# Optimization experiments

Measured on AMD Instinct MI355X. Metric: run time of the kernel, lower is better.

Reference implementation:

```python
import jax, jax.numpy as jnp
import numpy as np

D_MODEL = 1024
NUM_HEADS = 16
D_K = D_MODEL // NUM_HEADS


def setup_inputs() -> dict:
    key = jax.random.key(0)
    ks = jax.random.split(key, 12)
    B, S, D = 2, 2048, D_MODEL
    s = 1.0 / np.sqrt(D)
    inp = {
        "Q": jax.random.normal(ks[0], (B, S, D), jnp.float32),
        "K": jax.random.normal(ks[1], (B, S, D), jnp.float32),
        "V": jax.random.normal(ks[2], (B, S, D), jnp.float32),
        "Wq": jax.random.normal(ks[3], (D, D), jnp.float32) * s,
        "bq": jax.random.normal(ks[4], (D,), jnp.float32) * s,
        "Wk": jax.random.normal(ks[5], (D, D), jnp.float32) * s,
        "bk": jax.random.normal(ks[6], (D,), jnp.float32) * s,
        "Wv": jax.random.normal(ks[7], (D, D), jnp.float32) * s,
        "bv": jax.random.normal(ks[8], (D,), jnp.float32) * s,
        "Wo": jax.random.normal(ks[9], (D, D), jnp.float32) * s,
        "bo": jax.random.normal(ks[10], (D,), jnp.float32) * s,
    }
    return inp


def _split_heads(x, B, S):
    # [B, S, D] -> [B, H, S, d_k]
    return x.reshape(B, S, NUM_HEADS, D_K).transpose(0, 2, 1, 3)


def reference(Q, K, V, Wq, bq, Wk, bk, Wv, bv, Wo, bo):
    B, S, D = Q.shape
    # torch nn.Linear: y = x @ W.T + b
    q = _split_heads(Q @ Wq.T + bq, B, S)
    k = _split_heads(K @ Wk.T + bk, B, S)
    v = _split_heads(V @ Wv.T + bv, B, S)
    scale = 1.0 / np.sqrt(D_K).astype(np.float32)
    # [B, H, S, S] attention scores (materialized, as in the original)
    scores = jnp.einsum('bhqd,bhkd->bhqk', q, k) * scale
    probs = jax.nn.softmax(scores, axis=-1)
    out = jnp.einsum('bhqk,bhkd->bhqd', probs, v)
    out = out.transpose(0, 2, 1, 3).reshape(B, S, D)
    return out @ Wo.T + bo
```

## Files before the change

### kernel.cpp

```cpp
#include <hip/hip_runtime.h>
#include <hip/hip_bf16.h>

#define S_LEN   2048
#define NHEADS  16
#define DKH     64
#define DMODEL  1024
#define NBATCH  2

typedef __bf16 bf16x8 __attribute__((ext_vector_type(8)));
typedef __bf16 bf16x4 __attribute__((ext_vector_type(4)));
typedef float  f32x4  __attribute__((ext_vector_type(4)));

typedef __attribute__((address_space(3))) void       lds_void;
typedef const __attribute__((address_space(1))) void glob_void;

__device__ __forceinline__ void glds16(const void* g, void* l) {
    __builtin_amdgcn_global_load_lds((glob_void*)g, (lds_void*)l, 16, 0, 0);
}

struct CvtArgs {
    const float* src[7];
    __bf16*      dst[7];
    int          n[7];
};

__global__ __launch_bounds__(256)
void cvt_all_k(CvtArgs a)
{
    const int t = blockIdx.y;
    const size_t i = ((size_t)blockIdx.x * 256 + threadIdx.x) * 8;
    if ((int)i >= a.n[t]) return;
    const float* s = a.src[t];
    f32x4 lo = *(const f32x4*)(s + i);
    f32x4 hi = *(const f32x4*)(s + i + 4);
    bf16x8 r;
#pragma unroll
    for (int k = 0; k < 4; ++k) { r[k] = (__bf16)lo[k]; r[4 + k] = (__bf16)hi[k]; }
    *(bf16x8*)(a.dst[t] + i) = r;
}

__device__ __forceinline__ void gemm_core(
    const __bf16* __restrict__ A, const __bf16* __restrict__ W,
    int m0, int n0, int K,
    __bf16 (*As)[32], __bf16 (*Ws)[32], f32x4 acc[4][4])
{
    const int tid  = threadIdx.x;
    const int lane = tid & 63;
    const int wv   = tid >> 6;
    const int l15  = lane & 15;
    const int quad = lane >> 4;
    const int wm   = wv >> 1;
    const int wn   = wv & 1;
    const int grow = lane >> 2;
    const int gcol = (lane & 3) * 8;

    const __bf16* ag0 = A + (size_t)(m0 + wv * 32 + grow) * K + gcol;
    const __bf16* ag1 = A + (size_t)(m0 + wv * 32 + 16 + grow) * K + gcol;
    const __bf16* wg0 = W + (size_t)(n0 + wv * 32 + grow) * K + gcol;
    const __bf16* wg1 = W + (size_t)(n0 + wv * 32 + 16 + grow) * K + gcol;
    void* al0 = &As[wv * 32][0];
    void* al1 = &As[wv * 32 + 16][0];
    void* wl0 = &Ws[wv * 32][0];
    void* wl1 = &Ws[wv * 32 + 16][0];

    for (int k0 = 0;;) {
        __syncthreads();
        glds16(ag0 + k0, al0);
        glds16(ag1 + k0, al1);
        glds16(wg0 + k0, wl0);
        glds16(wg1 + k0, wl1);
        __syncthreads();

        bf16x8 af[4], wf[4];
#pragma unroll
        for (int i = 0; i < 4; ++i)
            af[i] = *(const bf16x8*)&As[wm * 64 + i * 16 + l15][quad * 8];
#pragma unroll
        for (int j = 0; j < 4; ++j)
            wf[j] = *(const bf16x8*)&Ws[wn * 64 + j * 16 + l15][quad * 8];
#pragma unroll
        for (int i = 0; i < 4; ++i)
#pragma unroll
            for (int j = 0; j < 4; ++j)
                acc[i][j] = __builtin_amdgcn_mfma_f32_16x16x32_bf16(af[i], wf[j], acc[i][j], 0, 0, 0);

        k0 += 32;
        if (k0 >= K) break;
    }
}

struct GArgs {
    const __bf16* A[3];
    const __bf16* W[3];
    const float*  bias[3];
    __bf16*       out[3];
};

__global__ __launch_bounds__(256)
void gemm_qkv(GArgs g, int z_off)
{
    __shared__ __align__(16) __bf16 As[128][32];
    __shared__ __align__(16) __bf16 Ws[128][32];

    const int fid = blockIdx.x;
    const int z   = (fid >> 8) + z_off;
    const int f8  = fid & 255;
    int m0, n0;
    if (z == 2) { m0 = (f8 & 7) * 128;  n0 = (f8 >> 3) * 128; }
    else        { m0 = (f8 & 31) * 128; n0 = (f8 >> 5) * 128; }

    f32x4 acc[4][4];
#pragma unroll
    for (int i = 0; i < 4; ++i)
#pragma unroll
        for (int j = 0; j < 4; ++j) acc[i][j] = (f32x4){0.f, 0.f, 0.f, 0.f};

    gemm_core(g.A[z], g.W[z], m0, n0, DMODEL, As, Ws, acc);

    const int lane = threadIdx.x & 63;
    const int wv   = threadIdx.x >> 6;
    const int l15  = lane & 15;
    const int quad = lane >> 4;
    const int wm   = wv >> 1;
    const int wn   = wv & 1;
    const float* bias = g.bias[z];
    __bf16* out = g.out[z];
    const float oscale = (z == 0) ? 0.125f : 1.0f;

#pragma unroll
    for (int j = 0; j < 4; ++j) {
        const int col = n0 + wn * 64 + j * 16 + l15;
        const float bcol = (z == 2) ? 0.f : bias[col];
#pragma unroll
        for (int i = 0; i < 4; ++i) {
#pragma unroll
            for (int r = 0; r < 4; ++r) {
                const int row = m0 + wm * 64 + i * 16 + quad * 4 + r;
                size_t idx;
                float v = acc[i][j][r];
                if (z == 2) {
                    const int h = row >> 6, d = row & (DKH - 1);
                    const int b = col >> 11, s = col & (S_LEN - 1);
                    v += bias[row];
                    idx = ((size_t)(b * NHEADS + h) * DKH + d) * S_LEN + s;
                } else {
                    const int b = row >> 11, s = row & (S_LEN - 1);
                    const int h = col >> 6, d = col & (DKH - 1);
                    v = (v + bcol) * oscale;
                    idx = ((size_t)(b * NHEADS + h) * S_LEN + s) * DKH + d;
                }
                out[idx] = (__bf16)v;
            }
        }
    }
}

__global__ __launch_bounds__(256)
void gemm_out(const __bf16* __restrict__ A, const __bf16* __restrict__ W,
              const float* __restrict__ bias, float* __restrict__ out)
{
    __shared__ __align__(16) __bf16 As[128][32];
    __shared__ __align__(16) __bf16 Ws[128][32];

    const int fid = blockIdx.x;
    const int m0 = (fid & 31) * 128;
    const int n0 = (fid >> 5) * 128;

    f32x4 acc[4][4];
#pragma unroll
    for (int i = 0; i < 4; ++i)
#pragma unroll
        for (int j = 0; j < 4; ++j) acc[i][j] = (f32x4){0.f, 0.f, 0.f, 0.f};

    gemm_core(A, W, m0, n0, DMODEL, As, Ws, acc);

    const int lane = threadIdx.x & 63;
    const int wv   = threadIdx.x >> 6;
    const int l15  = lane & 15;
    const int quad = lane >> 4;
    const int wm   = wv >> 1;
    const int wn   = wv & 1;

#pragma unroll
    for (int j = 0; j < 4; ++j) {
        const int col = n0 + wn * 64 + j * 16 + l15;
        const float bv = bias[col];
#pragma unroll
        for (int i = 0; i < 4; ++i)
#pragma unroll
            for (int r = 0; r < 4; ++r) {
                const int row = m0 + wm * 64 + i * 16 + quad * 4 + r;
                out[(size_t)row * DMODEL + col] = acc[i][j][r] + bv;
            }
    }
}

__global__ __launch_bounds__(512)
void attn_k(const __bf16* __restrict__ Qh, const __bf16* __restrict__ Kh,
            const __bf16* __restrict__ VhT, __bf16* __restrict__ out)
{
    __shared__ __align__(16) __bf16 Ks[128][72];
    __shared__ __align__(16) __bf16 Vs[64][136];

    const int tid  = threadIdx.x;
    const int lane = tid & 63;
    const int wv   = tid >> 6;
    const int l15  = lane & 15;
    const int quad = lane >> 4;

    const int fid = blockIdx.x;
    const int x  = fid & 7;
    const int j  = fid >> 3;
    const int bh = x * 4 + (j & 3);
    const int q0 = (j >> 2) * 128;
    const int b  = bh >> 4;
    const int h  = bh & (NHEADS - 1);

    const __bf16* Q  = Qh  + (size_t)bh * S_LEN * DKH;
    const __bf16* Kp = Kh  + (size_t)bh * S_LEN * DKH;
    const __bf16* Vt = VhT + (size_t)bh * DKH * S_LEN;

    const int qrow = q0 + wv * 16 + l15;
    const bf16x8 qa0 = *(const bf16x8*)(Q + (size_t)qrow * DKH + quad * 8);
    const bf16x8 qa1 = *(const bf16x8*)(Q + (size_t)qrow * DKH + quad * 8 + 32);

    const int krow = tid >> 2;
    const int kc0  = (tid & 3) * 16;
    const int vrow = tid >> 3;
    const int vc0  = (tid & 7) * 16;
    const __bf16* kst = Kp + (size_t)krow * DKH   + kc0;
    const __bf16* vst = Vt + (size_t)vrow * S_LEN + vc0;

    f32x4 oT[4];
#pragma unroll
    for (int jj = 0; jj < 4; ++jj) oT[jj] = (f32x4){0.f, 0.f, 0.f, 0.f};
    float lacc = 0.f;

    bf16x8 ka = *(const bf16x8*)(kst);
    bf16x8 kb = *(const bf16x8*)(kst + 8);
    bf16x8 va = *(const bf16x8*)(vst);
    bf16x8 vb = *(const bf16x8*)(vst + 8);

    for (int kt = 0; kt < S_LEN; kt += 128) {
        __syncthreads();
        *(bf16x8*)&Ks[krow][kc0]     = ka;
        *(bf16x8*)&Ks[krow][kc0 + 8] = kb;
        *(bf16x8*)&Vs[vrow][vc0]     = va;
        *(bf16x8*)&Vs[vrow][vc0 + 8] = vb;
        __syncthreads();
        if (kt + 128 < S_LEN) {
            ka = *(const bf16x8*)(kst + (size_t)(kt + 128) * DKH);
            kb = *(const bf16x8*)(kst + (size_t)(kt + 128) * DKH + 8);
            va = *(const bf16x8*)(vst + kt + 128);
            vb = *(const bf16x8*)(vst + kt + 128 + 8);
        }

#pragma unroll
        for (int ht = 0; ht < 2; ++ht) {
            float p[4][4];
#pragma unroll
            for (int n = 0; n < 4; ++n) {
                bf16x8 kA = *(const bf16x8*)&Ks[ht * 64 + n * 16 + l15][quad * 8];
                bf16x8 kB = *(const bf16x8*)&Ks[ht * 64 + n * 16 + l15][quad * 8 + 32];
                f32x4 st = {0.f, 0.f, 0.f, 0.f};
                st = __builtin_amdgcn_mfma_f32_16x16x32_bf16(kA, qa0, st, 0, 0, 0);
                st = __builtin_amdgcn_mfma_f32_16x16x32_bf16(kB, qa1, st, 0, 0, 0);
#pragma unroll
                for (int r = 0; r < 4; ++r) p[n][r] = __expf(st[r]);
            }
#pragma unroll
            for (int n = 0; n < 4; ++n)
#pragma unroll
                for (int r = 0; r < 4; ++r) lacc += p[n][r];

#pragma unroll
            for (int t = 0; t < 2; ++t) {
                bf16x8 pf;
#pragma unroll
                for (int jj = 0; jj < 4; ++jj) {
                    pf[jj]     = (__bf16)p[2 * t][jj];
                    pf[4 + jj] = (__bf16)p[2 * t + 1][jj];
                }
#pragma unroll
                for (int jt = 0; jt < 4; ++jt) {
                    bf16x4 v0 = *(const bf16x4*)&Vs[jt * 16 + l15][ht * 64 + t * 32 + quad * 4];
                    bf16x4 v1 = *(const bf16x4*)&Vs[jt * 16 + l15][ht * 64 + t * 32 + 16 + quad * 4];
                    bf16x8 vf;
#pragma unroll
                    for (int jj = 0; jj < 4; ++jj) { vf[jj] = v0[jj]; vf[4 + jj] = v1[jj]; }
                    oT[jt] = __builtin_amdgcn_mfma_f32_16x16x32_bf16(vf, pf, oT[jt], 0, 0, 0);
                }
            }
        }
    }

    lacc += __shfl_xor(lacc, 16);
    lacc += __shfl_xor(lacc, 32);
    const float inv = 1.0f / lacc;

    __bf16* op = out + ((size_t)b * S_LEN + q0 + wv * 16 + l15) * DMODEL + h * DKH;
#pragma unroll
    for (int jt = 0; jt < 4; ++jt) {
        bf16x4 t;
#pragma unroll
        for (int r = 0; r < 4; ++r) t[r] = (__bf16)(oT[jt][r] * inv);
        *(bf16x4*)(op + jt * 16 + quad * 4) = t;
    }
}

extern "C" void kernel_launch(void* const* d_in, const int* in_sizes, int n_in,
                              void* d_out, int out_size, void* d_ws, size_t ws_size,
                              hipStream_t stream) {
    const float* Qi = (const float*)d_in[0];
    const float* Ki = (const float*)d_in[1];
    const float* Vi = (const float*)d_in[2];
    const float* Wq = (const float*)d_in[3];
    const float* bq = (const float*)d_in[4];
    const float* Wk = (const float*)d_in[5];
    const float* bk = (const float*)d_in[6];
    const float* Wv = (const float*)d_in[7];
    const float* bv = (const float*)d_in[8];
    const float* Wo = (const float*)d_in[9];
    const float* bo = (const float*)d_in[10];
    float* out = (float*)d_out;

    const int M = NBATCH * S_LEN;
    const size_t NW = (size_t)DMODEL * DMODEL;
    const size_t NE = (size_t)M * DMODEL;
    const bool big = ws_size >= ((size_t)56 << 20);

    __bf16* w_bf   = (__bf16*)d_ws;
    __bf16* Qin_bf = w_bf + 4 * NW;
    __bf16* Kin_bf = Qin_bf + NE;
    __bf16* Vin_bf = Kin_bf + NE;
    __bf16* q_ws   = Vin_bf + NE;
    __bf16* k_ws   = q_ws + NE;
    __bf16* vT_ws   = big ? (k_ws + NE) : Kin_bf;
    __bf16* attn_ws = Qin_bf;
    __bf16* wq_bf = w_bf, *wk_bf = w_bf + NW, *wv_bf = w_bf + 2 * NW, *wo_bf = w_bf + 3 * NW;

    CvtArgs ca;
    ca.src[0] = Wq; ca.src[1] = Wk; ca.src[2] = Wv; ca.src[3] = Wo;
    ca.src[4] = Qi; ca.src[5] = Ki; ca.src[6] = Vi;
    ca.dst[0] = wq_bf; ca.dst[1] = wk_bf; ca.dst[2] = wv_bf; ca.dst[3] = wo_bf;
    ca.dst[4] = Qin_bf; ca.dst[5] = Kin_bf; ca.dst[6] = Vin_bf;
    for (int t = 0; t < 4; ++t) ca.n[t] = (int)NW;
    for (int t = 4; t < 7; ++t) ca.n[t] = (int)NE;
    cvt_all_k<<<dim3(2048, 7), 256, 0, stream>>>(ca);

    GArgs g;
    g.A[0] = Qin_bf; g.W[0] = wq_bf; g.bias[0] = bq; g.out[0] = q_ws;
    g.A[1] = Kin_bf; g.W[1] = wk_bf; g.bias[1] = bk; g.out[1] = k_ws;
    g.A[2] = wv_bf;  g.W[2] = Vin_bf; g.bias[2] = bv; g.out[2] = vT_ws;
    if (big) {
        gemm_qkv<<<dim3(768), 256, 0, stream>>>(g, 0);
    } else {
        gemm_qkv<<<dim3(512), 256, 0, stream>>>(g, 0);
        gemm_qkv<<<dim3(256), 256, 0, stream>>>(g, 2);
    }

    attn_k<<<dim3(512), dim3(512), 0, stream>>>(q_ws, k_ws, vT_ws, attn_ws);

    gemm_out<<<dim3(256), 256, 0, stream>>>(attn_ws, wo_bf, bo, out);
}
```

Before: 235.3 us.

## Give each attention wave two query tiles and swizzle GEMM block mapping

The attention kernel now runs 256 threads per block, with each wave handling 32 query rows (two 16-row tiles). This reuses every K and V fragment read from LDS across two MFMA chains. V is permuted in registers before the LDS store so each MFMA operand comes from a single 16-byte LDS read instead of two 8-byte reads. The GEMM kernels remap block IDs so groups of consecutive blocks share tiles, presumably to improve L2/XCD locality. The cost is fewer waves per block, higher register pressure from the doubled accumulators, and a different occupancy hint.

```diff
diff --git a/kernel.cpp b/kernel.cpp
--- a/kernel.cpp
+++ b/kernel.cpp
@@ -104,10 +104,12 @@
 
     const int fid = blockIdx.x;
     const int z   = (fid >> 8) + z_off;
-    const int f8  = fid & 255;
+    const int l   = fid & 255;
+    const int x   = l & 7;
+    const int t   = l >> 3;
     int m0, n0;
-    if (z == 2) { m0 = (f8 & 7) * 128;  n0 = (f8 >> 3) * 128; }
-    else        { m0 = (f8 & 31) * 128; n0 = (f8 >> 5) * 128; }
+    if (z == 2) { m0 = (t & 7) * 128;          n0 = (x * 4 + (t >> 3)) * 128; }
+    else        { m0 = (x * 4 + (t & 3)) * 128; n0 = (t >> 2) * 128; }
 
     f32x4 acc[4][4];
 #pragma unroll
@@ -163,8 +165,10 @@
     __shared__ __align__(16) __bf16 Ws[128][32];
 
     const int fid = blockIdx.x;
-    const int m0 = (fid & 31) * 128;
-    const int n0 = (fid >> 5) * 128;
+    const int x = fid & 7;
+    const int t = fid >> 3;
+    const int m0 = (x * 4 + (t & 3)) * 128;
+    const int n0 = (t >> 2) * 128;
 
     f32x4 acc[4][4];
 #pragma unroll
@@ -195,7 +199,7 @@
     }
 }
 
-__global__ __launch_bounds__(512)
+__global__ __launch_bounds__(256, 2)
 void attn_k(const __bf16* __restrict__ Qh, const __bf16* __restrict__ Kh,
             const __bf16* __restrict__ VhT, __bf16* __restrict__ out)
 {
@@ -220,91 +224,126 @@
     const __bf16* Kp = Kh  + (size_t)bh * S_LEN * DKH;
     const __bf16* Vt = VhT + (size_t)bh * DKH * S_LEN;
 
-    const int qrow = q0 + wv * 16 + l15;
-    const bf16x8 qa0 = *(const bf16x8*)(Q + (size_t)qrow * DKH + quad * 8);
-    const bf16x8 qa1 = *(const bf16x8*)(Q + (size_t)qrow * DKH + quad * 8 + 32);
-
-    const int krow = tid >> 2;
-    const int kc0  = (tid & 3) * 16;
-    const int vrow = tid >> 3;
-    const int vc0  = (tid & 7) * 16;
-    const __bf16* kst = Kp + (size_t)krow * DKH   + kc0;
-    const __bf16* vst = Vt + (size_t)vrow * S_LEN + vc0;
-
-    f32x4 oT[4];
-#pragma unroll
-    for (int jj = 0; jj < 4; ++jj) oT[jj] = (f32x4){0.f, 0.f, 0.f, 0.f};
-    float lacc = 0.f;
-
-    bf16x8 ka = *(const bf16x8*)(kst);
-    bf16x8 kb = *(const bf16x8*)(kst + 8);
-    bf16x8 va = *(const bf16x8*)(vst);
-    bf16x8 vb = *(const bf16x8*)(vst + 8);
+    bf16x8 qa[2][2];
+#pragma unroll
+    for (int u = 0; u < 2; ++u) {
+        const int qrow = q0 + wv * 32 + u * 16 + l15;
+        qa[u][0] = *(const bf16x8*)(Q + (size_t)qrow * DKH + quad * 8);
+        qa[u][1] = *(const bf16x8*)(Q + (size_t)qrow * DKH + quad * 8 + 32);
+    }
+
+    const int krow = tid >> 1, kcb = (tid & 1) * 32;
+    const int vrow = tid >> 2, vcb = (tid & 3) * 32;
+    const __bf16* kst = Kp + (size_t)krow * DKH   + kcb;
+    const __bf16* vst = Vt + (size_t)vrow * S_LEN + vcb;
+
+    f32x4 oT[2][4];
+#pragma unroll
+    for (int u = 0; u < 2; ++u)
+#pragma unroll
+        for (int jt = 0; jt < 4; ++jt) oT[u][jt] = (f32x4){0.f, 0.f, 0.f, 0.f};
+    float lacc[2] = {0.f, 0.f};
+
+    bf16x8 kreg[4], vperm[4];
+    {
+        bf16x8 vr[4];
+#pragma unroll
+        for (int p = 0; p < 4; ++p) {
+            kreg[p] = *(const bf16x8*)(kst + p * 8);
+            vr[p]   = *(const bf16x8*)(vst + p * 8);
+        }
+#pragma unroll
+        for (int p = 0; p < 4; ++p) {
+            const int G = (p >> 1), e = (p & 1) * 4;
+#pragma unroll
+            for (int s = 0; s < 4; ++s) {
+                vperm[p][s]     = vr[G][e + s];
+                vperm[p][4 + s] = vr[G + 2][e + s];
+            }
+        }
+    }
 
     for (int kt = 0; kt < S_LEN; kt += 128) {
         __syncthreads();
-        *(bf16x8*)&Ks[krow][kc0]     = ka;
-        *(bf16x8*)&Ks[krow][kc0 + 8] = kb;
-        *(bf16x8*)&Vs[vrow][vc0]     = va;
-        *(bf16x8*)&Vs[vrow][vc0 + 8] = vb;
+#pragma unroll
+        for (int p = 0; p < 4; ++p) {
+            *(bf16x8*)&Ks[krow][kcb + p * 8] = kreg[p];
+            *(bf16x8*)&Vs[vrow][vcb + p * 8] = vperm[p];
+        }
         __syncthreads();
         if (kt + 128 < S_LEN) {
-            ka = *(const bf16x8*)(kst + (size_t)(kt + 128) * DKH);
-            kb = *(const bf16x8*)(kst + (size_t)(kt + 128) * DKH + 8);
-            va = *(const bf16x8*)(vst + kt + 128);
-            vb = *(const bf16x8*)(vst + kt + 128 + 8);
+            bf16x8 vr[4];
+#pragma unroll
+            for (int p = 0; p < 4; ++p) {
+                kreg[p] = *(const bf16x8*)(kst + (size_t)(kt + 128) * DKH + p * 8);
+                vr[p]   = *(const bf16x8*)(vst + kt + 128 + p * 8);
+            }
+#pragma unroll
+            for (int p = 0; p < 4; ++p) {
+                const int G = (p >> 1), e = (p & 1) * 4;
+#pragma unroll
+                for (int s = 0; s < 4; ++s) {
+                    vperm[p][s]     = vr[G][e + s];
+                    vperm[p][4 + s] = vr[G + 2][e + s];
+                }
+            }
         }
 
 #pragma unroll
         for (int ht = 0; ht < 2; ++ht) {
-            float p[4][4];
+            float p[2][4][4];
 #pragma unroll
             for (int n = 0; n < 4; ++n) {
                 bf16x8 kA = *(const bf16x8*)&Ks[ht * 64 + n * 16 + l15][quad * 8];
                 bf16x8 kB = *(const bf16x8*)&Ks[ht * 64 + n * 16 + l15][quad * 8 + 32];
-                f32x4 st = {0.f, 0.f, 0.f, 0.f};
-                st = __builtin_amdgcn_mfma_f32_16x16x32_bf16(kA, qa0, st, 0, 0, 0);
-                st = __builtin_amdgcn_mfma_f32_16x16x32_bf16(kB, qa1, st, 0, 0, 0);
-#pragma unroll
-                for (int r = 0; r < 4; ++r) p[n][r] = __expf(st[r]);
-            }
-#pragma unroll
-            for (int n = 0; n < 4; ++n)
-#pragma unroll
-                for (int r = 0; r < 4; ++r) lacc += p[n][r];
+#pragma unroll
+                for (int u = 0; u < 2; ++u) {
+                    f32x4 st = {0.f, 0.f, 0.f, 0.f};
+                    st = __builtin_amdgcn_mfma_f32_16x16x32_bf16(kA, qa[u][0], st, 0, 0, 0);
+                    st = __builtin_amdgcn_mfma_f32_16x16x32_bf16(kB, qa[u][1], st, 0, 0, 0);
+#pragma unroll
+                    for (int r = 0; r < 4; ++r) {
+                        p[u][n][r] = __expf(st[r]);
+                        lacc[u] += p[u][n][r];
+                    }
+                }
+            }
 
 #pragma unroll
             for (int t = 0; t < 2; ++t) {
-                bf16x8 pf;
-#pragma unroll
-                for (int jj = 0; jj < 4; ++jj) {
-                    pf[jj]     = (__bf16)p[2 * t][jj];
-                    pf[4 + jj] = (__bf16)p[2 * t + 1][jj];
+                bf16x8 pf[2];
+#pragma unroll
+                for (int u = 0; u < 2; ++u)
+#pragma unroll
+                    for (int s = 0; s < 4; ++s) {
+                        pf[u][s]     = (__bf16)p[u][2 * t][s];
+                        pf[u][4 + s] = (__bf16)p[u][2 * t + 1][s];
+                    }
+#pragma unroll
+                for (int jt = 0; jt < 4; ++jt) {
+                    bf16x8 vf = *(const bf16x8*)&Vs[jt * 16 + l15][ht * 64 + t * 32 + quad * 8];
+#pragma unroll
+                    for (int u = 0; u < 2; ++u)
+                        oT[u][jt] = __builtin_amdgcn_mfma_f32_16x16x32_bf16(vf, pf[u], oT[u][jt], 0, 0, 0);
                 }
-#pragma unroll
-                for (int jt = 0; jt < 4; ++jt) {
-                    bf16x4 v0 = *(const bf16x4*)&Vs[jt * 16 + l15][ht * 64 + t * 32 + quad * 4];
-                    bf16x4 v1 = *(const bf16x4*)&Vs[jt * 16 + l15][ht * 64 + t * 32 + 16 + quad * 4];
-                    bf16x8 vf;
-#pragma unroll
-                    for (int jj = 0; jj < 4; ++jj) { vf[jj] = v0[jj]; vf[4 + jj] = v1[jj]; }
-                    oT[jt] = __builtin_amdgcn_mfma_f32_16x16x32_bf16(vf, pf, oT[jt], 0, 0, 0);
-                }
-            }
-        }
-    }
-
-    lacc += __shfl_xor(lacc, 16);
-    lacc += __shfl_xor(lacc, 32);
-    const float inv = 1.0f / lacc;
-
-    __bf16* op = out + ((size_t)b * S_LEN + q0 + wv * 16 + l15) * DMODEL + h * DKH;
-#pragma unroll
-    for (int jt = 0; jt < 4; ++jt) {
-        bf16x4 t;
-#pragma unroll
-        for (int r = 0; r < 4; ++r) t[r] = (__bf16)(oT[jt][r] * inv);
-        *(bf16x4*)(op + jt * 16 + quad * 4) = t;
+            }
+        }
+    }
+
+#pragma unroll
+    for (int u = 0; u < 2; ++u) {
+        float l = lacc[u];
+        l += __shfl_xor(l, 16);
+        l += __shfl_xor(l, 32);
+        const float inv = 1.0f / l;
+        __bf16* op = out + ((size_t)b * S_LEN + q0 + wv * 32 + u * 16 + l15) * DMODEL + h * DKH;
+#pragma unroll
+        for (int jt = 0; jt < 4; ++jt) {
+            bf16x4 t;
+#pragma unroll
+            for (int r = 0; r < 4; ++r) t[r] = (__bf16)(oT[u][jt][r] * inv);
+            *(bf16x4*)(op + jt * 16 + quad * 4) = t;
+        }
     }
 }
 
@@ -349,8 +388,8 @@
     cvt_all_k<<<dim3(2048, 7), 256, 0, stream>>>(ca);
 
     GArgs g;
-    g.A[0] = Qin_bf; g.W[0] = wq_bf; g.bias[0] = bq; g.out[0] = q_ws;
-    g.A[1] = Kin_bf; g.W[1] = wk_bf; g.bias[1] = bk; g.out[1] = k_ws;
+    g.A[0] = Qin_bf; g.W[0] = wq_bf;  g.bias[0] = bq; g.out[0] = q_ws;
+    g.A[1] = Kin_bf; g.W[1] = wk_bf;  g.bias[1] = bk; g.out[1] = k_ws;
     g.A[2] = wv_bf;  g.W[2] = Vin_bf; g.bias[2] = bv; g.out[2] = vT_ws;
     if (big) {
         gemm_qkv<<<dim3(768), 256, 0, stream>>>(g, 0);
@@ -359,7 +398,7 @@
         gemm_qkv<<<dim3(256), 256, 0, stream>>>(g, 2);
     }
 
-    attn_k<<<dim3(512), dim3(512), 0, stream>>>(q_ws, k_ws, vT_ws, attn_ws);
+    attn_k<<<dim3(512), 256, 0, stream>>>(q_ws, k_ws, vT_ws, attn_ws);
 
     gemm_out<<<dim3(256), 256, 0, stream>>>(attn_ws, wo_bf, bo, out);
 }
```

After: 246.3 us. 1.05x slower.
